# Kernel tuning notes

Hardware: AMD Instinct MI355X
Metric: run time of the kernel (lower is better)

Reference implementation:

```python
import jax, jax.numpy as jnp
import numpy as np

N, E, G = 100000, 800000, 64
F_IN, H = 92, 4
D1, D2, D3 = 32, 64, 128  # per-head out dims: hidden//2, hidden, 2*hidden
HID, LAT = 64, 128
FINAL = H * D3  # 512
NEG_SLOPE = 0.2


def _p(key, shape, scale=0.05):
    return jax.random.normal(key, shape, dtype=jnp.float32) * scale


def setup_inputs() -> dict:
    key = jax.random.key(0)
    ks = jax.random.split(key, 32)
    node_feat = jax.random.normal(ks[0], (N, F_IN), dtype=jnp.float32)
    src = jax.random.randint(ks[1], (E,), 0, N)
    dst = jax.random.randint(ks[2], (E,), 0, N)
    graph_id = jnp.sort(jax.random.randint(ks[3], (N,), 0, G))
    d = {"node_feat": node_feat, "src": src, "dst": dst, "graph_id": graph_id}
    # GAT layer params (DGL GATConv: fc no bias, attn_l/attn_r [H,D], bias [H*D])
    dims = [(F_IN, D1), (H * D1, D2), (H * D2, D3)]
    i = 4
    for li, (fi, do) in enumerate(dims, 1):
        d[f"W{li}"] = _p(ks[i], (fi, H * do)); i += 1
        d[f"al{li}"] = _p(ks[i], (H, do)); i += 1
        d[f"ar{li}"] = _p(ks[i], (H, do)); i += 1
        d[f"b{li}"] = jnp.zeros((H * do,), dtype=jnp.float32)
    # gate MLP: Linear(final, hid) -> ReLU -> Linear(hid, 1)
    d["Wg1"] = _p(ks[i], (FINAL, HID)); i += 1
    d["bg1"] = jnp.zeros((HID,), dtype=jnp.float32)
    d["Wg2"] = _p(ks[i], (HID, 1)); i += 1
    d["bg2"] = jnp.zeros((1,), dtype=jnp.float32)
    d["Wmu"] = _p(ks[i], (FINAL, LAT)); i += 1
    d["bmu"] = jnp.zeros((LAT,), dtype=jnp.float32)
    d["Wlv"] = _p(ks[i], (FINAL, LAT)); i += 1
    d["blv"] = jnp.zeros((LAT,), dtype=jnp.float32)
    return d


def gat_layer(h, W, al, ar, b, src, dst, heads, d_out):
    n = h.shape[0]
    Wh = (h @ W).reshape(n, heads, d_out)                      # [N,H,D]
    el = jnp.einsum('nhd,hd->nh', Wh, al)                      # a_l . Wh
    er = jnp.einsum('nhd,hd->nh', Wh, ar)
    e = jax.nn.leaky_relu(el[src] + er[dst], NEG_SLOPE)        # [E,H]
    m = jax.ops.segment_max(e, dst, num_segments=n)
    m = jnp.where(jnp.isfinite(m), m, 0.0)                     # zero-in-degree guard
    ex = jnp.exp(e - m[dst])
    s = jax.ops.segment_sum(ex, dst, num_segments=n)
    a = ex / jnp.maximum(s[dst], 1e-9)                         # edge softmax
    msg = a[:, :, None] * Wh[src]                              # [E,H,D] (peak intermediate)
    out = jax.ops.segment_sum(msg, dst, num_segments=n)        # scatter-aggregate
    out = out + b.reshape(1, heads, d_out)
    return out.reshape(n, heads * d_out)                       # flatten(1)


def attention_pool(h, graph_id, Wg1, bg1, Wg2, bg2, num_graphs):
    gate = jax.nn.relu(h @ Wg1 + bg1) @ Wg2 + bg2              # [N,1]
    m = jax.ops.segment_max(gate, graph_id, num_segments=num_graphs)
    ex = jnp.exp(gate - m[graph_id])
    s = jax.ops.segment_sum(ex, graph_id, num_segments=num_graphs)
    a = ex / jnp.maximum(s[graph_id], 1e-9)                    # softmax over nodes per graph
    return jax.ops.segment_sum(a * h, graph_id, num_segments=num_graphs)  # [G,final]


def reference(node_feat, src, dst, graph_id,
              W1, al1, ar1, b1, W2, al2, ar2, b2, W3, al3, ar3, b3,
              Wg1, bg1, Wg2, bg2, Wmu, bmu, Wlv, blv):
    h = jax.nn.elu(gat_layer(node_feat, W1, al1, ar1, b1, src, dst, H, D1))
    h = jax.nn.elu(gat_layer(h, W2, al2, ar2, b2, src, dst, H, D2))
    h = jax.nn.elu(gat_layer(h, W3, al3, ar3, b3, src, dst, H, D3))
    g = attention_pool(h, graph_id, Wg1, bg1, Wg2, bg2, G)
    mu = g @ Wmu + bmu
    logvar = g @ Wlv + blv
    return (mu, logvar)
```

## Files before the change

kernel.cpp:

```cpp
#include <hip/hip_runtime.h>
#include <math.h>

#define NNODES 100000
#define NEDGES 800000
#define NGRAPH 64
#define NHEAD  4
#define FINALD 512
#define HIDG   64
#define LATD   128
#define K1P    96
#define NB_SCAN 98
#define PQ     16

typedef unsigned int uint;
typedef unsigned short ushort;
typedef __attribute__((ext_vector_type(8))) short bf16x8;
typedef __attribute__((ext_vector_type(4))) float f32x4;

__device__ __forceinline__ float bflo(uint u) { return __uint_as_float(u << 16); }
__device__ __forceinline__ float bfhi(uint u) { return __uint_as_float(u & 0xffff0000u); }
__device__ __forceinline__ ushort f2bf(float f) {
    uint u = __float_as_uint(f);
    return (ushort)((u + 0x7fffu + ((u >> 16) & 1u)) >> 16);
}
__device__ __forceinline__ uint pack2(float a, float b) {
    return (uint)f2bf(a) | ((uint)f2bf(b) << 16);
}
__device__ __forceinline__ void fmabf2(float w, uint v, float& a0, float& a1) {
    a0 = fmaf(w, bflo(v), a0);
    a1 = fmaf(w, bfhi(v), a1);
}

__device__ __forceinline__ void async_copy16(const ushort* gsrc, ushort* lds_base) {
    __builtin_amdgcn_global_load_lds(
        (const __attribute__((address_space(1))) uint*)gsrc,
        (__attribute__((address_space(3))) uint*)lds_base,
        16, 0, 0);
}

__global__ void count_kernel(const int* __restrict__ dst, int* __restrict__ deg) {
    int e = blockIdx.x * blockDim.x + threadIdx.x;
    if (e < NEDGES) atomicAdd(&deg[dst[e]], 1);
}
__global__ __launch_bounds__(1024) void scan_block_kernel(const int* __restrict__ deg,
                                                          int* __restrict__ off,
                                                          int* __restrict__ bsum) {
    __shared__ int buf[1024];
    int t = threadIdx.x;
    int i = blockIdx.x * 1024 + t;
    int x = (i < NNODES) ? deg[i] : 0;
    buf[t] = x;
    __syncthreads();
    for (int s = 1; s < 1024; s <<= 1) {
        int v = (t >= s) ? buf[t - s] : 0;
        __syncthreads();
        buf[t] += v;
        __syncthreads();
    }
    if (i < NNODES) off[i] = buf[t] - x;
    if (t == 1023) bsum[blockIdx.x] = buf[1023];
}
__global__ __launch_bounds__(128) void scan_bsum_kernel(int* __restrict__ bsum) {
    __shared__ int buf[128];
    int t = threadIdx.x;
    int x = (t < NB_SCAN) ? bsum[t] : 0;
    buf[t] = x;
    __syncthreads();
    for (int s = 1; s < 128; s <<= 1) {
        int v = (t >= s) ? buf[t - s] : 0;
        __syncthreads();
        buf[t] += v;
        __syncthreads();
    }
    if (t < NB_SCAN) bsum[t] = buf[t] - x;
    if (t == 0) bsum[NB_SCAN] = buf[NB_SCAN - 1];
}
__global__ __launch_bounds__(1024) void scan_add_kernel(int* __restrict__ off,
                                                        const int* __restrict__ bsum,
                                                        int* __restrict__ cursor) {
    int i = blockIdx.x * 1024 + threadIdx.x;
    if (i < NNODES) {
        int v = off[i] + bsum[blockIdx.x];
        off[i] = v;
        cursor[i] = v;
    }
    if (i == 0) off[NNODES] = bsum[NB_SCAN];
}
__global__ void scatter_kernel(const int* __restrict__ src, const int* __restrict__ dst,
                               int* __restrict__ cursor, int* __restrict__ src_csr,
                               int* __restrict__ dst_csr) {
    int e = blockIdx.x * blockDim.x + threadIdx.x;
    if (e >= NEDGES) return;
    int d = dst[e];
    int p = atomicAdd(&cursor[d], 1);
    src_csr[p] = src[e];
    dst_csr[p] = d;
}

#define C1 (128 * K1P)
#define C2 (256 * 128)
#define C3 (512 * 256)
#define CG (64 * 512)
#define CX (NNODES * K1P)
#define CTOT (C1 + C2 + C3 + CG + CX + NNODES + NNODES + NGRAPH + 1)
__global__ void conv_all_kernel(const float* __restrict__ W1, const float* __restrict__ W2,
                                const float* __restrict__ W3, const float* __restrict__ Wg1,
                                const float* __restrict__ nf,
                                ushort* __restrict__ Bt1, ushort* __restrict__ Bt2,
                                ushort* __restrict__ Bt3, ushort* __restrict__ Btg,
                                ushort* __restrict__ x0, float* __restrict__ gate,
                                int* __restrict__ deg, const int* __restrict__ gid,
                                int* __restrict__ gstart) {
    int i = blockIdx.x * blockDim.x + threadIdx.x;
    if (i < C1) {
        int n = i / K1P, k = i - n * K1P;
        Bt1[i] = (k < 92) ? f2bf(W1[(size_t)k * 128 + n]) : (ushort)0;
        return;
    }
    i -= C1;
    if (i < C2) {
        int n = i >> 7, k = i & 127;
        Bt2[i] = f2bf(W2[(size_t)k * 256 + n]);
        return;
    }
    i -= C2;
    if (i < C3) {
        int n = i >> 8, k = i & 255;
        Bt3[i] = f2bf(W3[(size_t)k * 512 + n]);
        return;
    }
    i -= C3;
    if (i < CG) {
        int n = i >> 9, k = i & 511;
        Btg[i] = f2bf(Wg1[(size_t)k * 64 + n]);
        return;
    }
    i -= CG;
    if (i < CX) {
        int n = i / K1P, k = i - n * K1P;
        x0[i] = (k < 92) ? f2bf(nf[(size_t)n * 92 + k]) : (ushort)0;
        return;
    }
    i -= CX;
    if (i < NNODES) { gate[i] = 0.f; return; }
    i -= NNODES;
    if (i < NNODES) { deg[i] = 0; return; }
    i -= NNODES;
    if (i <= NGRAPH) {
        int lo = 0, hi = NNODES;
        while (lo < hi) {
            int mid = (lo + hi) >> 1;
            if (gid[mid] < i) lo = mid + 1; else hi = mid;
        }
        gstart[i] = lo;
    }
}

template <int BN, int MODE>
__global__ __launch_bounds__(256) void mfma_gemm(const ushort* __restrict__ A,
                                                 const ushort* __restrict__ Bt,
                                                 const float* __restrict__ bias,
                                                 ushort* __restrict__ C,
                                                 const float* __restrict__ Wg2,
                                                 float* __restrict__ gate,
                                                 int M, int K, int N) {
    constexpr int WNS = BN / 2;
    constexpr int NT = WNS / 16;
    __shared__ ushort Alds[128][32];
    __shared__ ushort Blds[BN][32];
    int tid = threadIdx.x;
    int wave = tid >> 6, lane = tid & 63;
    int wm = wave & 1, wn = wave >> 1;
    int quad = lane >> 4, l16 = lane & 15;
    int rowBase = blockIdx.y * 128;
    int colBase = blockIdx.x * BN;

    int srow = lane >> 2;
    int scol = (lane & 3) * 8;

    f32x4 acc[4][NT];
#pragma unroll
    for (int i = 0; i < 4; i++)
#pragma unroll
        for (int j = 0; j < NT; j++) acc[i][j] = (f32x4){0.f, 0.f, 0.f, 0.f};

    for (int k0 = 0; k0 < K; k0 += 32) {
#pragma unroll
        for (int c = 0; c < 2; c++) {
            int chunk = wave * 2 + c;
            int row = rowBase + chunk * 16 + srow;
            async_copy16(&A[(size_t)row * K + k0 + scol], &Alds[chunk * 16][0]);
        }
        if constexpr (BN == 128) {
#pragma unroll
            for (int c = 0; c < 2; c++) {
                int chunk = wave * 2 + c;
                int row = colBase + chunk * 16 + srow;
                async_copy16(&Bt[(size_t)row * K + k0 + scol], &Blds[chunk * 16][0]);
            }
        } else {
            int row = colBase + wave * 16 + srow;
            async_copy16(&Bt[(size_t)row * K + k0 + scol], &Blds[wave * 16][0]);
        }
        __syncthreads();
        bf16x8 af[4], bf[NT];
#pragma unroll
        for (int i = 0; i < 4; i++)
            af[i] = *(const bf16x8*)&Alds[wm * 64 + i * 16 + l16][quad * 8];
#pragma unroll
        for (int j = 0; j < NT; j++)
            bf[j] = *(const bf16x8*)&Blds[wn * WNS + j * 16 + l16][quad * 8];
#pragma unroll
        for (int i = 0; i < 4; i++)
#pragma unroll
            for (int j = 0; j < NT; j++)
                acc[i][j] = __builtin_amdgcn_mfma_f32_16x16x32_bf16(af[i], bf[j], acc[i][j], 0, 0, 0);
        __syncthreads();
    }

    if constexpr (MODE == 0) {
#pragma unroll
        for (int i = 0; i < 4; i++) {
#pragma unroll
            for (int j = 0; j < NT; j++) {
                int col = colBase + wn * WNS + j * 16 + l16;
#pragma unroll
                for (int r = 0; r < 4; r++) {
                    int row = rowBase + wm * 64 + i * 16 + quad * 4 + r;
                    if (row < M) C[(size_t)row * N + col] = f2bf(acc[i][j][r]);
                }
            }
        }
    } else {
        float bb[NT], wg[NT];
#pragma unroll
        for (int j = 0; j < NT; j++) {
            int col = colBase + wn * WNS + j * 16 + l16;
            bb[j] = bias[col];
            wg[j] = Wg2[col];
        }
#pragma unroll
        for (int i = 0; i < 4; i++) {
            float pd[4] = {0.f, 0.f, 0.f, 0.f};
#pragma unroll
            for (int j = 0; j < NT; j++) {
#pragma unroll
                for (int r = 0; r < 4; r++) {
                    float x = fmaxf(acc[i][j][r] + bb[j], 0.f);
                    pd[r] = fmaf(x, wg[j], pd[r]);
                }
            }
#pragma unroll
            for (int m = 1; m < 16; m <<= 1)
#pragma unroll
                for (int r = 0; r < 4; r++)
                    pd[r] += __shfl_xor(pd[r], m, 64);
            if (l16 == 0) {
#pragma unroll
                for (int r = 0; r < 4; r++) {
                    int row = rowBase + wm * 64 + i * 16 + quad * 4 + r;
                    if (row < M) atomicAdd(&gate[row], pd[r]);
                }
            }
        }
    }
}

template <int HD>
__global__ __launch_bounds__(256) void eler_node(const ushort* __restrict__ Wh,
                                                 const float* __restrict__ al,
                                                 const float* __restrict__ ar,
                                                 float* __restrict__ el,
                                                 float* __restrict__ er) {
    constexpr int LPN = HD / 8;
    constexpr int NPW = 64 / LPN;
    constexpr int S = (HD / NHEAD) / 8;
    int wave = threadIdx.x >> 6;
    int lane = threadIdx.x & 63;
    int sub = lane & (LPN - 1);
    int n = blockIdx.x * (4 * NPW) + wave * NPW + lane / LPN;
    int d0 = sub * 8;
    uint4 v = *(const uint4*)&Wh[(size_t)n * HD + d0];
    float w0 = bflo(v.x), w1 = bfhi(v.x), w2 = bflo(v.y), w3 = bfhi(v.y);
    float w4 = bflo(v.z), w5 = bfhi(v.z), w6 = bflo(v.w), w7 = bfhi(v.w);
    float4 a0 = *(const float4*)&al[d0];
    float4 a1 = *(const float4*)&al[d0 + 4];
    float4 b0 = *(const float4*)&ar[d0];
    float4 b1 = *(const float4*)&ar[d0 + 4];
    float sl, sr;
    sl = w0 * a0.x; sl = fmaf(w1, a0.y, sl); sl = fmaf(w2, a0.z, sl); sl = fmaf(w3, a0.w, sl);
    sl = fmaf(w4, a1.x, sl); sl = fmaf(w5, a1.y, sl); sl = fmaf(w6, a1.z, sl); sl = fmaf(w7, a1.w, sl);
    sr = w0 * b0.x; sr = fmaf(w1, b0.y, sr); sr = fmaf(w2, b0.z, sr); sr = fmaf(w3, b0.w, sr);
    sr = fmaf(w4, b1.x, sr); sr = fmaf(w5, b1.y, sr); sr = fmaf(w6, b1.z, sr); sr = fmaf(w7, b1.w, sr);
#pragma unroll
    for (int o = S / 2; o > 0; o >>= 1) {
        sl += __shfl_down(sl, o, 64);
        sr += __shfl_down(sr, o, 64);
    }
    if ((sub & (S - 1)) == 0) {
        int h = sub / S;
        el[n * 4 + h] = sl;
        er[n * 4 + h] = sr;
    }
}

__global__ void attn_edge(const int* __restrict__ src_csr, const int* __restrict__ dst_csr,
                          const float4* __restrict__ el4, const float4* __restrict__ er4,
                          float4* __restrict__ aw4) {
    int i = blockIdx.x * blockDim.x + threadIdx.x;
    if (i >= NEDGES) return;
    int s = src_csr[i];
    int d = dst_csr[i];
    float4 a = el4[s];
    float4 b = er4[d];
    float x0 = a.x + b.x, x1 = a.y + b.y, x2 = a.z + b.z, x3 = a.w + b.w;
    x0 = (x0 >= 0.f) ? x0 : 0.2f * x0;
    x1 = (x1 >= 0.f) ? x1 : 0.2f * x1;
    x2 = (x2 >= 0.f) ? x2 : 0.2f * x2;
    x3 = (x3 >= 0.f) ? x3 : 0.2f * x3;
    float4 w;
    w.x = expf(x0 - 8.f); w.y = expf(x1 - 8.f);
    w.z = expf(x2 - 8.f); w.w = expf(x3 - 8.f);
    aw4[i] = w;
}

template <int HD, int DPL>
__global__ __launch_bounds__(256) void gat_aggregate2(const int* __restrict__ src_csr,
                                                      const int* __restrict__ off,
                                                      const ushort* __restrict__ Wh,
                                                      const float* __restrict__ aw,
                                                      const float* __restrict__ bias,
                                                      ushort* __restrict__ out,
                                                      int pass) {
    constexpr int LOGD = (HD == 128) ? 5 : (HD == 256) ? 6 : 7;
    const int lane = threadIdx.x & 63;
    const int wv = __builtin_amdgcn_readfirstlane((int)(threadIdx.x >> 6));
    const int n = blockIdx.x * 4 + wv;
    const int d = pass * (64 * DPL) + lane * DPL;
    const int h = d >> LOGD;
    const int i0 = __builtin_amdgcn_readfirstlane(off[n]);
    const int i1 = __builtin_amdgcn_readfirstlane(off[n + 1]);

    float a0 = 0.f, a1 = 0.f, a2 = 0.f, a3 = 0.f;
    float ssum = 0.f;
    const ushort* __restrict__ col = Wh + d;

    int i = i0;
    for (; i + 4 <= i1; i += 4) {
        const int s0 = __builtin_amdgcn_readfirstlane(src_csr[i + 0]);
        const int s1 = __builtin_amdgcn_readfirstlane(src_csr[i + 1]);
        const int s2 = __builtin_amdgcn_readfirstlane(src_csr[i + 2]);
        const int s3 = __builtin_amdgcn_readfirstlane(src_csr[i + 3]);
        const float w0 = aw[(i + 0) * 4 + h];
        const float w1 = aw[(i + 1) * 4 + h];
        const float w2 = aw[(i + 2) * 4 + h];
        const float w3 = aw[(i + 3) * 4 + h];
        ssum += w0; ssum += w1; ssum += w2; ssum += w3;
        if constexpr (DPL == 4) {
            uint2 v0 = *(const uint2*)&col[(size_t)s0 * HD];
            uint2 v1 = *(const uint2*)&col[(size_t)s1 * HD];
            uint2 v2 = *(const uint2*)&col[(size_t)s2 * HD];
            uint2 v3 = *(const uint2*)&col[(size_t)s3 * HD];
            fmabf2(w0, v0.x, a0, a1); fmabf2(w0, v0.y, a2, a3);
            fmabf2(w1, v1.x, a0, a1); fmabf2(w1, v1.y, a2, a3);
            fmabf2(w2, v2.x, a0, a1); fmabf2(w2, v2.y, a2, a3);
            fmabf2(w3, v3.x, a0, a1); fmabf2(w3, v3.y, a2, a3);
        } else {
            uint v0 = *(const uint*)&col[(size_t)s0 * HD];
            uint v1 = *(const uint*)&col[(size_t)s1 * HD];
            uint v2 = *(const uint*)&col[(size_t)s2 * HD];
            uint v3 = *(const uint*)&col[(size_t)s3 * HD];
            fmabf2(w0, v0, a0, a1);
            fmabf2(w1, v1, a0, a1);
            fmabf2(w2, v2, a0, a1);
            fmabf2(w3, v3, a0, a1);
        }
    }
    for (; i < i1; ++i) {
        const int s0 = __builtin_amdgcn_readfirstlane(src_csr[i]);
        const float w0 = aw[i * 4 + h];
        ssum += w0;
        if constexpr (DPL == 4) {
            uint2 v0 = *(const uint2*)&col[(size_t)s0 * HD];
            fmabf2(w0, v0.x, a0, a1); fmabf2(w0, v0.y, a2, a3);
        } else {
            uint v0 = *(const uint*)&col[(size_t)s0 * HD];
            fmabf2(w0, v0, a0, a1);
        }
    }

    const float inv = 1.f / fmaxf(ssum, 1e-9f);
    float x0 = a0 * inv + bias[d + 0];
    float x1 = a1 * inv + bias[d + 1];
    x0 = (x0 > 0.f) ? x0 : (expf(x0) - 1.f);
    x1 = (x1 > 0.f) ? x1 : (expf(x1) - 1.f);
    if constexpr (DPL == 4) {
        float x2 = a2 * inv + bias[d + 2];
        float x3 = a3 * inv + bias[d + 3];
        x2 = (x2 > 0.f) ? x2 : (expf(x2) - 1.f);
        x3 = (x3 > 0.f) ? x3 : (expf(x3) - 1.f);
        uint2 o;
        o.x = pack2(x0, x1);
        o.y = pack2(x2, x3);
        *(uint2*)&out[(size_t)n * HD + d] = o;
    } else {
        *(uint*)&out[(size_t)n * HD + d] = pack2(x0, x1);
    }
}

__global__ __launch_bounds__(128) void pool_partial(const ushort* __restrict__ h,
                                                    const float* __restrict__ gate,
                                                    const int* __restrict__ gstart,
                                                    float* __restrict__ partial) {
    int g = blockIdx.x, q = blockIdx.y;
    int n0 = gstart[g], n1 = gstart[g + 1];
    __shared__ float red[128];
    int t = threadIdx.x;
    float m = -1e30f;
    for (int n = n0 + t; n < n1; n += 128) m = fmaxf(m, gate[n]);
    red[t] = m; __syncthreads();
    for (int s = 64; s > 0; s >>= 1) {
        if (t < s) red[t] = fmaxf(red[t], red[t + s]);
        __syncthreads();
    }
    m = red[0];

    int len = n1 - n0;
    int chunk = (len + PQ - 1) / PQ;
    int s = n0 + q * chunk;
    int e = s + chunk; if (e > n1) e = n1;
    int d4 = t;
    const uint2* h2 = (const uint2*)h;
    float a0 = 0.f, a1 = 0.f, a2 = 0.f, a3 = 0.f;
    for (int n = s; n < e; n++) {
        float w = expf(gate[n] - m);
        uint2 v = h2[(size_t)n * 128 + d4];
        a0 = fmaf(w, bflo(v.x), a0);
        a1 = fmaf(w, bfhi(v.x), a1);
        a2 = fmaf(w, bflo(v.y), a2);
        a3 = fmaf(w, bfhi(v.y), a3);
    }
    *(float4*)&partial[((size_t)(g * PQ + q)) * FINALD + d4 * 4] = make_float4(a0, a1, a2, a3);
}

__global__ __launch_bounds__(128) void final_kernel(const float* __restrict__ partial,
                                                    const float* __restrict__ gate,
                                                    const int* __restrict__ gstart,
                                                    const float* __restrict__ Wmu,
                                                    const float* __restrict__ bmu,
                                                    const float* __restrict__ Wlv,
                                                    const float* __restrict__ blv,
                                                    float* __restrict__ out) {
    int g = blockIdx.x, j = threadIdx.x;
    int n0 = gstart[g], n1 = gstart[g + 1];
    __shared__ float red[128];
    __shared__ float pooled[FINALD];
    float m = -1e30f;
    for (int n = n0 + j; n < n1; n += 128) m = fmaxf(m, gate[n]);
    red[j] = m; __syncthreads();
    for (int s = 64; s > 0; s >>= 1) {
        if (j < s) red[j] = fmaxf(red[j], red[j + s]);
        __syncthreads();
    }
    m = red[0]; __syncthreads();
    float sum = 0.f;
    for (int n = n0 + j; n < n1; n += 128) sum += expf(gate[n] - m);
    red[j] = sum; __syncthreads();
    for (int s = 64; s > 0; s >>= 1) {
        if (j < s) red[j] += red[j + s];
        __syncthreads();
    }
    float gsum = red[0];

    const float* p = partial + (size_t)g * PQ * FINALD;
    for (int k = j; k < FINALD; k += 128) {
        float v = 0.f;
#pragma unroll
        for (int q = 0; q < PQ; q++) v += p[q * FINALD + k];
        pooled[k] = v;
    }
    __syncthreads();
    float am = 0.f, av = 0.f;
    for (int k = 0; k < FINALD; k++) {
        float pv = pooled[k];
        am = fmaf(pv, Wmu[k * LATD + j], am);
        av = fmaf(pv, Wlv[k * LATD + j], av);
    }
    float inv = 1.f / fmaxf(gsum, 1e-9f);
    out[g * LATD + j] = am * inv + bmu[j];
    out[NGRAPH * LATD + g * LATD + j] = av * inv + blv[j];
}

extern "C" void kernel_launch(void* const* d_in, const int* in_sizes, int n_in,
                              void* d_out, int out_size, void* d_ws, size_t ws_size,
                              hipStream_t stream) {
    (void)in_sizes; (void)n_in; (void)out_size; (void)ws_size;
    const float* node_feat = (const float*)d_in[0];
    const int* src = (const int*)d_in[1];
    const int* dst = (const int*)d_in[2];
    const int* gid = (const int*)d_in[3];
    const float* W[3]    = {(const float*)d_in[4],  (const float*)d_in[8],  (const float*)d_in[12]};
    const float* al[3]   = {(const float*)d_in[5],  (const float*)d_in[9],  (const float*)d_in[13]};
    const float* ar[3]   = {(const float*)d_in[6],  (const float*)d_in[10], (const float*)d_in[14]};
    const float* bias[3] = {(const float*)d_in[7],  (const float*)d_in[11], (const float*)d_in[15]};
    const float* Wg1 = (const float*)d_in[16];
    const float* bg1 = (const float*)d_in[17];
    const float* Wg2 = (const float*)d_in[18];
    const float* Wmu = (const float*)d_in[20];
    const float* bmu = (const float*)d_in[21];
    const float* Wlv = (const float*)d_in[22];
    const float* blv = (const float*)d_in[23];

    char* ws = (char*)d_ws;
    size_t woff = 0;
    auto carve = [&](size_t bytes) {
        void* p = ws + woff;
        woff = (woff + bytes + 255) & ~(size_t)255;
        return p;
    };
    ushort* hA      = (ushort*)carve((size_t)NNODES * 512 * 2);
    ushort* hB      = (ushort*)carve((size_t)NNODES * 512 * 2);
    float*  el      = (float*) carve((size_t)NNODES * 4 * 4);
    float*  er      = (float*) carve((size_t)NNODES * 4 * 4);
    float*  aw      = (float*) carve((size_t)NEDGES * 4 * 4);
    int*    deg     = (int*)   carve((size_t)NNODES * 4);
    int*    off     = (int*)   carve((size_t)(NNODES + 1) * 4);
    int*    cursor  = (int*)   carve((size_t)NNODES * 4);
    int*    src_csr = (int*)   carve((size_t)NEDGES * 4);
    int*    dst_csr = (int*)   carve((size_t)NEDGES * 4);
    int*    bsum    = (int*)   carve((size_t)(NB_SCAN + 1) * 4);
    float*  gate    = (float*) carve((size_t)NNODES * 4);
    int*    gstart  = (int*)   carve((size_t)(NGRAPH + 1) * 4);
    float*  partial = (float*) carve((size_t)NGRAPH * PQ * FINALD * 4);
    ushort* Bt1     = (ushort*)carve((size_t)128 * K1P * 2);
    ushort* Bt2     = (ushort*)carve((size_t)256 * 128 * 2);
    ushort* Bt3     = (ushort*)carve((size_t)512 * 256 * 2);
    ushort* Btg     = (ushort*)carve((size_t)64 * 512 * 2 + 4096);
    ushort* x0      = hA;

    conv_all_kernel<<<(CTOT + 255) / 256, 256, 0, stream>>>(
        W[0], W[1], W[2], Wg1, node_feat, Bt1, Bt2, Bt3, Btg, x0, gate, deg, gid, gstart);
    count_kernel<<<(NEDGES + 255) / 256, 256, 0, stream>>>(dst, deg);
    scan_block_kernel<<<NB_SCAN, 1024, 0, stream>>>(deg, off, bsum);
    scan_bsum_kernel<<<1, 128, 0, stream>>>(bsum);
    scan_add_kernel<<<NB_SCAN, 1024, 0, stream>>>(off, bsum, cursor);
    scatter_kernel<<<(NEDGES + 255) / 256, 256, 0, stream>>>(src, dst, cursor, src_csr, dst_csr);

    const int MB = (NNODES + 127) / 128;
    const int AGB = NNODES / 4;
    const int EB = (NEDGES + 255) / 256;

    mfma_gemm<128, 0><<<dim3(1, MB), 256, 0, stream>>>(
        x0, Bt1, nullptr, hB, nullptr, nullptr, NNODES, K1P, 128);
    eler_node<128><<<NNODES / 16, 256, 0, stream>>>(hB, al[0], ar[0], el, er);
    attn_edge<<<EB, 256, 0, stream>>>(
        src_csr, dst_csr, (const float4*)el, (const float4*)er, (float4*)aw);
    gat_aggregate2<128, 2><<<AGB, 256, 0, stream>>>(
        src_csr, off, hB, aw, bias[0], hA, 0);

    mfma_gemm<128, 0><<<dim3(2, MB), 256, 0, stream>>>(
        hA, Bt2, nullptr, hB, nullptr, nullptr, NNODES, 128, 256);
    eler_node<256><<<NNODES / 8, 256, 0, stream>>>(hB, al[1], ar[1], el, er);
    attn_edge<<<EB, 256, 0, stream>>>(
        src_csr, dst_csr, (const float4*)el, (const float4*)er, (float4*)aw);
    gat_aggregate2<256, 4><<<AGB, 256, 0, stream>>>(
        src_csr, off, hB, aw, bias[1], hA, 0);

    mfma_gemm<128, 0><<<dim3(4, MB), 256, 0, stream>>>(
        hA, Bt3, nullptr, hB, nullptr, nullptr, NNODES, 256, 512);
    eler_node<512><<<NNODES / 4, 256, 0, stream>>>(hB, al[2], ar[2], el, er);
    attn_edge<<<EB, 256, 0, stream>>>(
        src_csr, dst_csr, (const float4*)el, (const float4*)er, (float4*)aw);
    gat_aggregate2<512, 4><<<AGB, 256, 0, stream>>>(
        src_csr, off, hB, aw, bias[2], hA, 0);
    gat_aggregate2<512, 4><<<AGB, 256, 0, stream>>>(
        src_csr, off, hB, aw, bias[2], hA, 1);

    mfma_gemm<64, 1><<<dim3(1, MB), 256, 0, stream>>>(
        hA, Btg, bg1, nullptr, Wg2, gate, NNODES, FINALD, HIDG);
    pool_partial<<<dim3(NGRAPH, PQ), 128, 0, stream>>>(hA, gate, gstart, partial);
    final_kernel<<<NGRAPH, 128, 0, stream>>>(partial, gate, gstart, Wmu, bmu, Wlv, blv, (float*)d_out);
}
```

Baseline: 720.0 us.

## Double GEMM K-tile to 64 with XOR-swizzled LDS layout

The MFMA GEMM now stages 64-wide K slices per iteration instead of 32, halving barrier count and loop overhead. LDS rows are XOR-swizzled in 16-byte chunks so the fragment reads avoid bank conflicts. Layer-1 K padding goes from 96 to 128 to match the new tile, which adds zero-padded work and extra input conversion traffic for the first GEMM.

After: 722.1 us. Within noise of the previous version (+0.3%).

```diff
diff --git a/kernel.cpp b/kernel.cpp
--- a/kernel.cpp
+++ b/kernel.cpp
@@ -8,7 +8,7 @@
 #define FINALD 512
 #define HIDG   64
 #define LATD   128
-#define K1P    96
+#define K1P    128
 #define NB_SCAN 98
 #define PQ     16
 
@@ -113,7 +113,7 @@
                                 int* __restrict__ gstart) {
     int i = blockIdx.x * blockDim.x + threadIdx.x;
     if (i < C1) {
-        int n = i / K1P, k = i - n * K1P;
+        int n = i >> 7, k = i & 127;
         Bt1[i] = (k < 92) ? f2bf(W1[(size_t)k * 128 + n]) : (ushort)0;
         return;
     }
@@ -137,7 +137,7 @@
     }
     i -= CG;
     if (i < CX) {
-        int n = i / K1P, k = i - n * K1P;
+        int n = i >> 7, k = i & 127;
         x0[i] = (k < 92) ? f2bf(nf[(size_t)n * 92 + k]) : (ushort)0;
         return;
     }
@@ -166,8 +166,8 @@
                                                  int M, int K, int N) {
     constexpr int WNS = BN / 2;
     constexpr int NT = WNS / 16;
-    __shared__ ushort Alds[128][32];
-    __shared__ ushort Blds[BN][32];
+    __shared__ ushort Alds[128][64];
+    __shared__ ushort Blds[BN][64];
     int tid = threadIdx.x;
     int wave = tid >> 6, lane = tid & 63;
     int wm = wave & 1, wn = wave >> 1;
@@ -175,8 +175,10 @@
     int rowBase = blockIdx.y * 128;
     int colBase = blockIdx.x * BN;
 
-    int srow = lane >> 2;
-    int scol = (lane & 3) * 8;
+    int srow8 = lane >> 3;
+    int scol = ((lane & 7) ^ srow8) * 8;
+    int rp0 = ((quad) ^ (l16 & 7)) * 8;
+    int rp1 = ((4 + quad) ^ (l16 & 7)) * 8;
 
     f32x4 acc[4][NT];
 #pragma unroll
@@ -184,37 +186,57 @@
 #pragma unroll
         for (int j = 0; j < NT; j++) acc[i][j] = (f32x4){0.f, 0.f, 0.f, 0.f};
 
-    for (int k0 = 0; k0 < K; k0 += 32) {
-#pragma unroll
-        for (int c = 0; c < 2; c++) {
-            int chunk = wave * 2 + c;
-            int row = rowBase + chunk * 16 + srow;
-            async_copy16(&A[(size_t)row * K + k0 + scol], &Alds[chunk * 16][0]);
+    for (int k0 = 0; k0 < K; k0 += 64) {
+#pragma unroll
+        for (int c = 0; c < 4; c++) {
+            int chunk = wave * 4 + c;
+            int row = rowBase + chunk * 8 + srow8;
+            async_copy16(&A[(size_t)row * K + k0 + scol], &Alds[chunk * 8][0]);
         }
         if constexpr (BN == 128) {
+#pragma unroll
+            for (int c = 0; c < 4; c++) {
+                int chunk = wave * 4 + c;
+                int row = colBase + chunk * 8 + srow8;
+                async_copy16(&Bt[(size_t)row * K + k0 + scol], &Blds[chunk * 8][0]);
+            }
+        } else {
 #pragma unroll
             for (int c = 0; c < 2; c++) {
                 int chunk = wave * 2 + c;
-                int row = colBase + chunk * 16 + srow;
-                async_copy16(&Bt[(size_t)row * K + k0 + scol], &Blds[chunk * 16][0]);
+                int row = colBase + chunk * 8 + srow8;
+                async_copy16(&Bt[(size_t)row * K + k0 + scol], &Blds[chunk * 8][0]);
             }
-        } else {
-            int row = colBase + wave * 16 + srow;
-            async_copy16(&Bt[(size_t)row * K + k0 + scol], &Blds[wave * 16][0]);
-        }
-        __syncthreads();
-        bf16x8 af[4], bf[NT];
-#pragma unroll
-        for (int i = 0; i < 4; i++)
-            af[i] = *(const bf16x8*)&Alds[wm * 64 + i * 16 + l16][quad * 8];
-#pragma unroll
-        for (int j = 0; j < NT; j++)
-            bf[j] = *(const bf16x8*)&Blds[wn * WNS + j * 16 + l16][quad * 8];
-#pragma unroll
-        for (int i = 0; i < 4; i++)
+        }
+        __syncthreads();
+        {
+            bf16x8 af[4], bf[NT];
+#pragma unroll
+            for (int i = 0; i < 4; i++)
+                af[i] = *(const bf16x8*)&Alds[wm * 64 + i * 16 + l16][rp0];
 #pragma unroll
             for (int j = 0; j < NT; j++)
-                acc[i][j] = __builtin_amdgcn_mfma_f32_16x16x32_bf16(af[i], bf[j], acc[i][j], 0, 0, 0);
+                bf[j] = *(const bf16x8*)&Blds[wn * WNS + j * 16 + l16][rp0];
+#pragma unroll
+            for (int i = 0; i < 4; i++)
+#pragma unroll
+                for (int j = 0; j < NT; j++)
+                    acc[i][j] = __builtin_amdgcn_mfma_f32_16x16x32_bf16(af[i], bf[j], acc[i][j], 0, 0, 0);
+        }
+        {
+            bf16x8 af[4], bf[NT];
+#pragma unroll
+            for (int i = 0; i < 4; i++)
+                af[i] = *(const bf16x8*)&Alds[wm * 64 + i * 16 + l16][rp1];
+#pragma unroll
+            for (int j = 0; j < NT; j++)
+                bf[j] = *(const bf16x8*)&Blds[wn * WNS + j * 16 + l16][rp1];
+#pragma unroll
+            for (int i = 0; i < 4; i++)
+#pragma unroll
+                for (int j = 0; j < NT; j++)
+                    acc[i][j] = __builtin_amdgcn_mfma_f32_16x16x32_bf16(af[i], bf[j], acc[i][j], 0, 0, 0);
+        }
         __syncthreads();
     }
 
```
